# Kernel optimization log

Hardware: AMD Instinct MI355X
Metric: run time of the kernel (lower is better)

Reference implementation:

```python
import jax, jax.numpy as jnp
import numpy as np
from jax import lax

K = 2000      # node_num of GraphConvolution
H, W = 75, 100  # edge_region_feature spatial grid (from per-pixel concat loops)


def setup_inputs() -> dict:
    key = jax.random.key(0)
    k1, k2, k3, k4 = jax.random.split(key, 4)
    b, c = 8, 512
    edge_region_feature = jax.random.normal(k1, (b, c, H, W), dtype=jnp.float32)
    edge_region_predict = jax.random.normal(k2, (b, 3, H, W), dtype=jnp.float32)
    # GraphConvolution params: kaiming_normal_(fan_out) weights, zero bias
    w1 = jax.random.normal(k3, (512, 128), dtype=jnp.float32) * np.sqrt(2.0 / 128)
    b1 = jnp.zeros((K, 128), dtype=jnp.float32)
    w2 = jax.random.normal(k4, (128, 128), dtype=jnp.float32) * np.sqrt(2.0 / 128)
    b2 = jnp.zeros((K, 128), dtype=jnp.float32)
    return {"edge_region_feature": edge_region_feature,
            "edge_region_predict": edge_region_predict,
            "w1": w1, "b1": b1, "w2": w2, "b2": b2}


def reference(edge_region_feature, edge_region_predict, w1, b1, w2, b2):
    b, c = edge_region_feature.shape[0], edge_region_feature.shape[1]
    # block_feature built as: for x in range(W) for y in range(H) -> node n at (y=n%H, x=n//H)
    block = jnp.transpose(edge_region_feature, (0, 3, 2, 1)).reshape(b, W * H, c)  # (b, 7500, 512)

    # topk over channel-0 prediction, flattened row-major (idx = y*W + x)
    scores = edge_region_predict[:, 0, :, :].reshape(b, -1)            # (b, 7500)
    _vals, topk_idx = lax.top_k(scores, K)
    sorted_idx = jnp.sort(topk_idx, axis=1)                            # (b, 2000) int32

    # gather node features (replicates original's indexing of block_feature)
    node_map = jnp.take_along_axis(block, sorted_idx[:, :, None], axis=1)  # (b, 2000, 512)

    # generate_adjacent_map: decode positions with width=W, connect 8-neighborhood (+self)
    py = sorted_idx // W
    px = sorted_idx % W
    near_y = jnp.abs(py[:, :, None] - py[:, None, :]) <= 1
    near_x = jnp.abs(px[:, :, None] - px[:, None, :]) <= 1
    adj = (near_y & near_x).astype(jnp.float32)                        # (b, 2000, 2000)

    # node_feature_grouping = ReLU6 -> GCN(512->128) -> GCN(128->128)
    inp = jnp.clip(jnp.concatenate([adj, node_map], axis=2), 0.0, 6.0)  # ReLU6 on cat(adj, nodes)
    a = inp[:, :, :K]
    nf = inp[:, :, K:]
    # GCN1: A @ X @ W1 + b1  (in!=out -> no residual)
    x1 = jnp.einsum('bij,bjf->bif', a, nf) @ w1 + b1                   # (b, 2000, 128)
    # GCN2: A @ X1 @ W2 + b2 + X1 (in==out -> residual)
    x2 = jnp.einsum('bij,bjf->bif', a, x1) @ w2 + b2 + x1              # (b, 2000, 128)

    node_output_feature = jnp.tanh(x2)
    return node_output_feature, sorted_idx
```

## Files before the change

### kernel.cpp

```cpp
#include <hip/hip_runtime.h>
#include <cmath>

#define H_DIM 75
#define W_DIM 100
#define HW 7500
#define KSEL 2000
#define BATCH 8
#define CIN 512
#define FDIM 128

typedef short v4s __attribute__((ext_vector_type(4)));
typedef short v8s __attribute__((ext_vector_type(8)));
typedef float v16f __attribute__((ext_vector_type(16)));

__device__ __forceinline__ unsigned int map_key(float f) {
  unsigned int u = __float_as_uint(f);
  return (u & 0x80000000u) ? ~u : (u | 0x80000000u);
}

__device__ __forceinline__ float fast_tanh(float x) {
  float e = __expf(2.0f * x);
  return 1.0f - 2.0f * __builtin_amdgcn_rcpf(e + 1.0f);
}

__device__ __forceinline__ unsigned short bf16_rne(float v) {
  unsigned int u = __float_as_uint(v);
  unsigned int r = u + 0x7FFFu + ((u >> 16) & 1u);
  return (unsigned short)(r >> 16);
}
__device__ __forceinline__ float bf16_to_f(unsigned short h) {
  return __uint_as_float(((unsigned int)h) << 16);
}

__global__ __launch_bounds__(1024) void topk_nbr_kernel(
    const float* __restrict__ pred, const float* __restrict__ w1,
    const float* __restrict__ w2,
    int* __restrict__ off2_ws, int* __restrict__ perm_ws,
    float* __restrict__ out_idx,
    unsigned short* __restrict__ nbr, unsigned char* __restrict__ cnt,
    unsigned short* __restrict__ w1t_hi, unsigned short* __restrict__ w1t_lo,
    unsigned short* __restrict__ w2t_hi, unsigned short* __restrict__ w2t_lo)
{
  __shared__ unsigned int keys[HW];
  __shared__ unsigned int whist[16 * 256];
  __shared__ unsigned int hist[256];
  __shared__ unsigned int partials[16];
  __shared__ unsigned int s_prefix, s_kth;
  const int tid = threadIdx.x;

  if (blockIdx.x >= BATCH) {
    int base = (blockIdx.x - BATCH) * 1024 + tid;
    for (int e = base; e < CIN * FDIM + FDIM * FDIM; e += 8 * 1024) {
      if (e < CIN * FDIM) {
        int k = e & (CIN - 1), f = e >> 9;
        float v = w1[k * FDIM + f];
        unsigned short hi = bf16_rne(v);
        unsigned short lo = bf16_rne(v - bf16_to_f(hi));
        w1t_hi[(size_t)f * CIN + k] = hi;
        w1t_lo[(size_t)f * CIN + k] = lo;
      } else {
        int e2 = e - CIN * FDIM;
        int k = e2 & (FDIM - 1), f = e2 >> 7;
        float v = w2[k * FDIM + f];
        unsigned short hi = bf16_rne(v);
        unsigned short lo = bf16_rne(v - bf16_to_f(hi));
        w2t_hi[(size_t)f * FDIM + k] = hi;
        w2t_lo[(size_t)f * FDIM + k] = lo;
      }
    }
    return;
  }

  const int b = blockIdx.x;
  const int lane = tid & 63, w = tid >> 6;
  const float* scores = pred + (size_t)b * 3 * HW;
  for (int i = tid; i < HW; i += 1024) keys[i] = map_key(scores[i]);
  if (tid == 0) { s_prefix = 0u; s_kth = KSEL; }
  __syncthreads();

  for (int shift = 24; shift >= 0; shift -= 8) {
    for (int i = tid; i < 16 * 256; i += 1024) whist[i] = 0u;
    __syncthreads();
    unsigned int pref = s_prefix;
    unsigned int maskhi = (shift == 24) ? 0u : (0xFFFFFFFFu << (shift + 8));
    for (int i = tid; i < HW; i += 1024) {
      unsigned int k = keys[i];
      if ((k & maskhi) == pref)
        atomicAdd(&whist[w * 256 + ((k >> shift) & 0xFFu)], 1u);
    }
    __syncthreads();
    if (tid < 256) {
      unsigned int s = 0;
      #pragma unroll
      for (int ww = 0; ww < 16; ++ww) s += whist[ww * 256 + tid];
      hist[tid] = s;
    }
    __syncthreads();
    if (tid < 64) {
      unsigned int b0 = hist[tid * 4], b1 = hist[tid * 4 + 1];
      unsigned int b2 = hist[tid * 4 + 2], b3 = hist[tid * 4 + 3];
      unsigned int kth = s_kth;
      unsigned int T = b0 + b1 + b2 + b3;
      #pragma unroll
      for (int off = 1; off < 64; off <<= 1) {
        unsigned int t = __shfl_down(T, off, 64);
        if (tid + off < 64) T += t;
      }
      unsigned int U = __shfl_down(T, 1, 64);
      if (tid == 63) U = 0u;
      unsigned int s3 = b3 + U, s2 = b2 + s3, s1 = b1 + s2, s0 = b0 + s1;
      if (s0 >= kth && s1 < kth) { s_prefix = pref | ((unsigned)(4 * tid + 0) << shift); s_kth = kth - s1; }
      if (s1 >= kth && s2 < kth) { s_prefix = pref | ((unsigned)(4 * tid + 1) << shift); s_kth = kth - s2; }
      if (s2 >= kth && s3 < kth) { s_prefix = pref | ((unsigned)(4 * tid + 2) << shift); s_kth = kth - s3; }
      if (s3 >= kth && U  < kth) { s_prefix = pref | ((unsigned)(4 * tid + 3) << shift); s_kth = kth - U; }
    }
    __syncthreads();
  }
  const unsigned int thresh = s_prefix;

  unsigned int local[8];
  unsigned int sum = 0;
  #pragma unroll
  for (int e = 0; e < 8; ++e) {
    int i = tid * 8 + e;
    unsigned int p = 0;
    if (i < HW) {
      unsigned int ky = keys[i];
      if (ky > thresh) p = 1u;
      else if (ky == thresh) p = (1u << 16);
    }
    local[e] = p; sum += p;
  }
  __syncthreads();
  short* pos_of  = (short*)keys;
  int*   s_idx_sh = (int*)((char*)keys + 15000);
  for (int i = tid; i < HW; i += 1024) pos_of[i] = -1;

  unsigned int inc = sum;
  #pragma unroll
  for (int off = 1; off < 64; off <<= 1) {
    unsigned int t = __shfl_up(inc, off, 64);
    if (lane >= off) inc += t;
  }
  if (lane == 63) partials[w] = inc;
  __syncthreads();
  if (tid < 16) {
    unsigned int v = partials[tid];
    #pragma unroll
    for (int off = 1; off < 16; off <<= 1) {
      unsigned int t = __shfl_up(v, off, 64);
      if (tid >= off) v += t;
    }
    partials[tid] = v;
  }
  __syncthreads();
  unsigned int total = partials[15];
  unsigned int run = (w ? partials[w - 1] : 0u) + inc - sum;
  unsigned int ties = (unsigned int)KSEL - (total & 0xFFFFu);
  #pragma unroll
  for (int e = 0; e < 8; ++e) {
    int i = tid * 8 + e;
    unsigned int p = local[e];
    unsigned int gt_pref = run & 0xFFFFu;
    unsigned int eq_pref = run >> 16;
    bool sel = (p & 1u) || (((p >> 16) != 0u) && eq_pref < ties);
    if (sel) {
      unsigned int pos = gt_pref + (eq_pref < ties ? eq_pref : ties);
      out_idx[b * KSEL + pos] = (float)i;
      s_idx_sh[pos] = i;
      pos_of[i] = (short)pos;
    }
    run += p;
  }
  __syncthreads();

  if (tid < 128) hist[tid] = 0u;
  __syncthreads();
  for (int pos = tid; pos < KSEL; pos += 1024)
    atomicAdd(&hist[s_idx_sh[pos] % H_DIM], 1u);
  __syncthreads();
  if (tid == 0) {
    unsigned int run2 = 0u;
    for (int j = 0; j < H_DIM; ++j) { unsigned int t = hist[j]; hist[j] = run2; run2 += t; }
  }
  __syncthreads();
  for (int pos = tid; pos < KSEL; pos += 1024) {
    int i = s_idx_sh[pos];
    int y = i % H_DIM;
    unsigned int j = atomicAdd(&hist[y], 1u);
    off2_ws[b * KSEL + j] = (i % H_DIM) * W_DIM + i / H_DIM;
    perm_ws[b * KSEL + j] = pos;
  }

  for (int i = tid; i < KSEL; i += 1024) {
    int q = s_idx_sh[i];
    int py = q / W_DIM, px = q % W_DIM;
    unsigned short tmp[9];
    int c = 0;
    #pragma unroll
    for (int dy = -1; dy <= 1; ++dy) {
      int y = py + dy;
      if ((unsigned)y >= (unsigned)H_DIM) continue;
      #pragma unroll
      for (int dx = -1; dx <= 1; ++dx) {
        int x = px + dx;
        if ((unsigned)x >= (unsigned)W_DIM) continue;
        short p = pos_of[y * W_DIM + x];
        if (p >= 0) tmp[c++] = (unsigned short)p;
      }
    }
    #pragma unroll
    for (int t = 0; t < 9; ++t)
      nbr[(size_t)(b * KSEL + i) * 9 + t] = (t < c) ? tmp[t] : (unsigned short)0;
    cnt[b * KSEL + i] = (unsigned char)c;
  }
}

__global__ __launch_bounds__(256) void gemm1_fused(
    const float* __restrict__ feat, const int* __restrict__ off2_ws,
    const int* __restrict__ perm_ws,
    const unsigned short* __restrict__ w1t_hi,
    const unsigned short* __restrict__ w1t_lo,
    float* __restrict__ G)
{
  __shared__ unsigned short a_hi[3][64][20], a_lo[3][64][20];
  const int b = blockIdx.y;
  const int n0 = blockIdx.x * 64;
  const int tid = threadIdx.x;
  const int lane = tid & 63, w = tid >> 6;
  const int wr = w & 1, wc = w >> 1;
  const int q = lane >> 5, m = lane & 31;
  v16f acc0, acc1;
  #pragma unroll
  for (int i = 0; i < 16; ++i) { acc0[i] = 0.f; acc1[i] = 0.f; }
  const int an = wr * 32 + m;
  const int f0 = wc * 64 + m;
  const int n_st = tid & 63, ks = (tid >> 6) * 4;
  int nidx = n0 + n_st;
  if (nidx > KSEL - 1) nidx = KSEL - 1;
  const float* fb = feat + (size_t)b * CIN * HW + off2_ws[b * KSEL + nidx];

  float rv[3][4];
  #pragma unroll
  for (int s = 0; s < 3; ++s)
    #pragma unroll
    for (int j = 0; j < 4; ++j)
      rv[s][j] = fb[(size_t)(s * 16 + ks + j) * HW];
  #pragma unroll
  for (int j = 0; j < 4; ++j) {
    float v = fminf(fmaxf(rv[0][j], 0.f), 6.f);
    unsigned short hi = bf16_rne(v);
    a_hi[0][n_st][ks + j] = hi;
    a_lo[0][n_st][ks + j] = bf16_rne(v - bf16_to_f(hi));
  }

  #pragma unroll
  for (int i = 0; i < 32; ++i) {
    if (i + 1 < 32) {
      const int s = (i + 1) % 3;
      #pragma unroll
      for (int j = 0; j < 4; ++j) {
        float v = fminf(fmaxf(rv[s][j], 0.f), 6.f);
        unsigned short hi = bf16_rne(v);
        a_hi[s][n_st][ks + j] = hi;
        a_lo[s][n_st][ks + j] = bf16_rne(v - bf16_to_f(hi));
      }
      if (i + 3 < 32) {
        #pragma unroll
        for (int j = 0; j < 4; ++j)
          rv[s][j] = fb[(size_t)((i + 3) * 16 + ks + j) * HW];
      }
    }
    __syncthreads();
    const int p = i % 3;
    const int k0 = i * 16;
    v4s ah0 = *(const v4s*)&a_hi[p][an][q * 8];
    v4s ah1 = *(const v4s*)&a_hi[p][an][q * 8 + 4];
    v4s al0 = *(const v4s*)&a_lo[p][an][q * 8];
    v4s al1 = *(const v4s*)&a_lo[p][an][q * 8 + 4];
    v8s avh = __builtin_shufflevector(ah0, ah1, 0, 1, 2, 3, 4, 5, 6, 7);
    v8s avl = __builtin_shufflevector(al0, al1, 0, 1, 2, 3, 4, 5, 6, 7);
    v8s b0h = *(const v8s*)&w1t_hi[(size_t)f0 * CIN + k0 + q * 8];
    v8s b0l = *(const v8s*)&w1t_lo[(size_t)f0 * CIN + k0 + q * 8];
    v8s b1h = *(const v8s*)&w1t_hi[(size_t)(f0 + 32) * CIN + k0 + q * 8];
    v8s b1l = *(const v8s*)&w1t_lo[(size_t)(f0 + 32) * CIN + k0 + q * 8];
    acc0 = __builtin_amdgcn_mfma_f32_32x32x16_bf16(avh, b0h, acc0, 0, 0, 0);
    acc0 = __builtin_amdgcn_mfma_f32_32x32x16_bf16(avh, b0l, acc0, 0, 0, 0);
    acc0 = __builtin_amdgcn_mfma_f32_32x32x16_bf16(avl, b0h, acc0, 0, 0, 0);
    acc1 = __builtin_amdgcn_mfma_f32_32x32x16_bf16(avh, b1h, acc1, 0, 0, 0);
    acc1 = __builtin_amdgcn_mfma_f32_32x32x16_bf16(avh, b1l, acc1, 0, 0, 0);
    acc1 = __builtin_amdgcn_mfma_f32_32x32x16_bf16(avl, b1h, acc1, 0, 0, 0);
  }
  float* ob = G + (size_t)b * KSEL * FDIM;
  const int* pb = perm_ws + b * KSEL;
  #pragma unroll
  for (int reg = 0; reg < 16; ++reg) {
    int row = n0 + wr * 32 + (reg & 3) + 8 * (reg >> 2) + 4 * q;
    if (row < KSEL) {
      int pr = pb[row];
      ob[(size_t)pr * FDIM + f0]      = acc0[reg];
      ob[(size_t)pr * FDIM + f0 + 32] = acc1[reg];
    }
  }
}

__global__ __launch_bounds__(256) void gemm2_fused(
    const float* __restrict__ G, const float* __restrict__ b1,
    const unsigned short* __restrict__ nbr, const unsigned char* __restrict__ cnt,
    const unsigned short* __restrict__ w2t_hi,
    const unsigned short* __restrict__ w2t_lo,
    float* __restrict__ x1, float* __restrict__ Hm)
{
  __shared__ __align__(16) unsigned short xh[64][FDIM];
  __shared__ __align__(16) unsigned short xl[64][FDIM];
  const int b = blockIdx.y;
  const int n0 = blockIdx.x * 64;
  const int tid = threadIdx.x;
  const int g = tid >> 5, lane32 = tid & 31;
  const float4* G4 = (const float4*)G + (size_t)b * KSEL * 32;

  #pragma unroll 2
  for (int rr = 0; rr < 8; ++rr) {
    const int r = rr * 8 + g;
    const int node = n0 + r;
    const int nodec = (node > KSEL - 1) ? KSEL - 1 : node;
    const size_t bi = (size_t)b * KSEL + nodec;
    const unsigned short* nb = nbr + bi * 9;
    unsigned short idx[9];
    #pragma unroll
    for (int t = 0; t < 9; ++t) idx[t] = nb[t];
    const int c = cnt[bi];
    float4 v[9];
    #pragma unroll
    for (int t = 0; t < 9; ++t) v[t] = G4[(size_t)idx[t] * 32 + lane32];
    float4 acc = ((const float4*)b1)[nodec * 32 + lane32];
    #pragma unroll
    for (int t = 0; t < 9; ++t) {
      float mk = (t < c) ? 1.f : 0.f;
      acc.x = fmaf(v[t].x, mk, acc.x);
      acc.y = fmaf(v[t].y, mk, acc.y);
      acc.z = fmaf(v[t].z, mk, acc.z);
      acc.w = fmaf(v[t].w, mk, acc.w);
    }
    if (node < KSEL) ((float4*)x1)[bi * 32 + lane32] = acc;
    ushort4 h, l;
    h.x = bf16_rne(acc.x); l.x = bf16_rne(acc.x - bf16_to_f(h.x));
    h.y = bf16_rne(acc.y); l.y = bf16_rne(acc.y - bf16_to_f(h.y));
    h.z = bf16_rne(acc.z); l.z = bf16_rne(acc.z - bf16_to_f(h.z));
    h.w = bf16_rne(acc.w); l.w = bf16_rne(acc.w - bf16_to_f(h.w));
    const int cs = (lane32 * 4) ^ ((r & 15) << 3);
    *(ushort4*)&xh[r][cs] = h;
    *(ushort4*)&xl[r][cs] = l;
  }
  __syncthreads();

  const int lane = tid & 63, w = tid >> 6;
  const int wr = w & 1, wc = w >> 1;
  const int q = lane >> 5, m = lane & 31;
  const int ar = wr * 32 + m;
  const int f0 = wc * 64 + m;
  v16f acc0, acc1;
  #pragma unroll
  for (int i = 0; i < 16; ++i) { acc0[i] = 0.f; acc1[i] = 0.f; }
  #pragma unroll
  for (int k0 = 0; k0 < FDIM; k0 += 16) {
    const int ac = (k0 + q * 8) ^ ((ar & 15) << 3);
    v8s avh = *(const v8s*)&xh[ar][ac];
    v8s avl = *(const v8s*)&xl[ar][ac];
    v8s b0h = *(const v8s*)&w2t_hi[(size_t)f0 * FDIM + k0 + q * 8];
    v8s b0l = *(const v8s*)&w2t_lo[(size_t)f0 * FDIM + k0 + q * 8];
    v8s b1h = *(const v8s*)&w2t_hi[(size_t)(f0 + 32) * FDIM + k0 + q * 8];
    v8s b1l = *(const v8s*)&w2t_lo[(size_t)(f0 + 32) * FDIM + k0 + q * 8];
    acc0 = __builtin_amdgcn_mfma_f32_32x32x16_bf16(avh, b0h, acc0, 0, 0, 0);
    acc0 = __builtin_amdgcn_mfma_f32_32x32x16_bf16(avh, b0l, acc0, 0, 0, 0);
    acc0 = __builtin_amdgcn_mfma_f32_32x32x16_bf16(avl, b0h, acc0, 0, 0, 0);
    acc1 = __builtin_amdgcn_mfma_f32_32x32x16_bf16(avh, b1h, acc1, 0, 0, 0);
    acc1 = __builtin_amdgcn_mfma_f32_32x32x16_bf16(avh, b1l, acc1, 0, 0, 0);
    acc1 = __builtin_amdgcn_mfma_f32_32x32x16_bf16(avl, b1h, acc1, 0, 0, 0);
  }
  float* ob = Hm + (size_t)b * KSEL * FDIM;
  #pragma unroll
  for (int reg = 0; reg < 16; ++reg) {
    int row = n0 + wr * 32 + (reg & 3) + 8 * (reg >> 2) + 4 * q;
    if (row < KSEL) {
      ob[(size_t)row * FDIM + f0]      = acc0[reg];
      ob[(size_t)row * FDIM + f0 + 32] = acc1[reg];
    }
  }
}

__global__ __launch_bounds__(256) void out_kernel(
    const float* __restrict__ Hm, const float* __restrict__ x1,
    const float* __restrict__ b2,
    const unsigned short* __restrict__ nbr, const unsigned char* __restrict__ cnt,
    float* __restrict__ out)
{
  const int g = threadIdx.x >> 5, lane = threadIdx.x & 31;
  const int node = blockIdx.x * 8 + g;
  const int bb = blockIdx.y;
  const size_t bi = (size_t)bb * KSEL + node;
  const unsigned short* nb = nbr + bi * 9;
  unsigned short idx[9];
  #pragma unroll
  for (int t = 0; t < 9; ++t) idx[t] = nb[t];
  const int c = cnt[bi];
  const float4* H4 = (const float4*)Hm + (size_t)bb * KSEL * 32;
  float4 v[9];
  #pragma unroll
  for (int t = 0; t < 9; ++t) v[t] = H4[(size_t)idx[t] * 32 + lane];
  float4 acc = ((const float4*)b2)[node * 32 + lane];
  float4 xv = ((const float4*)x1)[bi * 32 + lane];
  acc.x += xv.x; acc.y += xv.y; acc.z += xv.z; acc.w += xv.w;
  #pragma unroll
  for (int t = 0; t < 9; ++t) {
    float mk = (t < c) ? 1.f : 0.f;
    acc.x = fmaf(v[t].x, mk, acc.x);
    acc.y = fmaf(v[t].y, mk, acc.y);
    acc.z = fmaf(v[t].z, mk, acc.z);
    acc.w = fmaf(v[t].w, mk, acc.w);
  }
  float4 r;
  r.x = fast_tanh(acc.x); r.y = fast_tanh(acc.y);
  r.z = fast_tanh(acc.z); r.w = fast_tanh(acc.w);
  ((float4*)out)[bi * 32 + lane] = r;
}

extern "C" void kernel_launch(void* const* d_in, const int* in_sizes, int n_in,
                              void* d_out, int out_size, void* d_ws, size_t ws_size,
                              hipStream_t stream) {
  const float* feat = (const float*)d_in[0];
  const float* pred = (const float*)d_in[1];
  const float* w1   = (const float*)d_in[2];
  const float* b1   = (const float*)d_in[3];
  const float* w2   = (const float*)d_in[4];
  const float* b2   = (const float*)d_in[5];
  float* out0 = (float*)d_out;
  float* out_idx = out0 + (size_t)BATCH * KSEL * FDIM;

  char* ws = (char*)d_ws;
  int*            off2_ws = (int*)(ws + 0);
  int*            perm_ws = (int*)(ws + 64256);
  unsigned short* nbr     = (unsigned short*)(ws + 128512);
  unsigned char*  cnt     = (unsigned char*)(ws + 416512);
  float*          G       = (float*)(ws + 432640);
  float*          x1      = (float*)(ws + 8624640);
  float*          Hm      = (float*)(ws + 16816640);
  unsigned short* w1t_hi  = (unsigned short*)(ws + 25008640);
  unsigned short* w1t_lo  = (unsigned short*)(ws + 25139712);
  unsigned short* w2t_hi  = (unsigned short*)(ws + 25270784);
  unsigned short* w2t_lo  = (unsigned short*)(ws + 25303552);

  topk_nbr_kernel<<<BATCH + 8, 1024, 0, stream>>>(
      pred, w1, w2, off2_ws, perm_ws, out_idx, nbr, cnt,
      w1t_hi, w1t_lo, w2t_hi, w2t_lo);
  gemm1_fused<<<dim3(32, BATCH), 256, 0, stream>>>(
      feat, off2_ws, perm_ws, w1t_hi, w1t_lo, G);
  gemm2_fused<<<dim3(32, BATCH), 256, 0, stream>>>(G, b1, nbr, cnt, w2t_hi, w2t_lo, x1, Hm);
  out_kernel<<<dim3(KSEL / 8, BATCH), 256, 0, stream>>>(Hm, x1, b2, nbr, cnt, out0);
}
```

Baseline: 233.5 us.

## Restructure gemm1 to single-wave blocks loading A fragments directly into registers

The gather GEMM now uses one 64-lane wave per block covering 32 nodes and all 128 output features. Each lane loads its A fragment straight from global memory into registers, with a 4-deep register prefetch. This removes the shared-memory staging and the per-iteration __syncthreads, and roughly doubles the block count (63x8 instead of 32x8) to spread work across more CUs. In exchange each wave holds four accumulators, raising register pressure, and each loaded feature value is converted to the hi/lo split only once per lane.

```diff
diff --git a/kernel.cpp b/kernel.cpp
--- a/kernel.cpp
+++ b/kernel.cpp
@@ -216,90 +216,71 @@
   }
 }
 
-__global__ __launch_bounds__(256) void gemm1_fused(
+__global__ __launch_bounds__(64) void gemm1_fused(
     const float* __restrict__ feat, const int* __restrict__ off2_ws,
     const int* __restrict__ perm_ws,
     const unsigned short* __restrict__ w1t_hi,
     const unsigned short* __restrict__ w1t_lo,
     float* __restrict__ G)
 {
-  __shared__ unsigned short a_hi[3][64][20], a_lo[3][64][20];
   const int b = blockIdx.y;
-  const int n0 = blockIdx.x * 64;
-  const int tid = threadIdx.x;
-  const int lane = tid & 63, w = tid >> 6;
-  const int wr = w & 1, wc = w >> 1;
+  const int n0 = blockIdx.x * 32;
+  const int lane = threadIdx.x;
   const int q = lane >> 5, m = lane & 31;
-  v16f acc0, acc1;
-  #pragma unroll
-  for (int i = 0; i < 16; ++i) { acc0[i] = 0.f; acc1[i] = 0.f; }
-  const int an = wr * 32 + m;
-  const int f0 = wc * 64 + m;
-  const int n_st = tid & 63, ks = (tid >> 6) * 4;
-  int nidx = n0 + n_st;
+  int nidx = n0 + m;
   if (nidx > KSEL - 1) nidx = KSEL - 1;
   const float* fb = feat + (size_t)b * CIN * HW + off2_ws[b * KSEL + nidx];
 
-  float rv[3][4];
-  #pragma unroll
-  for (int s = 0; s < 3; ++s)
-    #pragma unroll
-    for (int j = 0; j < 4; ++j)
-      rv[s][j] = fb[(size_t)(s * 16 + ks + j) * HW];
-  #pragma unroll
-  for (int j = 0; j < 4; ++j) {
-    float v = fminf(fmaxf(rv[0][j], 0.f), 6.f);
-    unsigned short hi = bf16_rne(v);
-    a_hi[0][n_st][ks + j] = hi;
-    a_lo[0][n_st][ks + j] = bf16_rne(v - bf16_to_f(hi));
-  }
+  v16f acc[4];
+  #pragma unroll
+  for (int c = 0; c < 4; ++c)
+    #pragma unroll
+    for (int i = 0; i < 16; ++i) acc[c][i] = 0.f;
+
+  float va[4][8];
+  #pragma unroll
+  for (int s = 0; s < 4; ++s)
+    #pragma unroll
+    for (int j = 0; j < 8; ++j)
+      va[s][j] = fb[(size_t)(s * 16 + q * 8 + j) * HW];
 
   #pragma unroll
   for (int i = 0; i < 32; ++i) {
-    if (i + 1 < 32) {
-      const int s = (i + 1) % 3;
+    const int s = i & 3;
+    v8s avh, avl;
+    #pragma unroll
+    for (int j = 0; j < 8; ++j) {
+      float v = fminf(fmaxf(va[s][j], 0.f), 6.f);
+      unsigned short hi = bf16_rne(v);
+      avh[j] = (short)hi;
+      avl[j] = (short)bf16_rne(v - bf16_to_f(hi));
+    }
+    if (i + 4 < 32) {
       #pragma unroll
-      for (int j = 0; j < 4; ++j) {
-        float v = fminf(fmaxf(rv[s][j], 0.f), 6.f);
-        unsigned short hi = bf16_rne(v);
-        a_hi[s][n_st][ks + j] = hi;
-        a_lo[s][n_st][ks + j] = bf16_rne(v - bf16_to_f(hi));
-      }
-      if (i + 3 < 32) {
-        #pragma unroll
-        for (int j = 0; j < 4; ++j)
-          rv[s][j] = fb[(size_t)((i + 3) * 16 + ks + j) * HW];
-      }
-    }
-    __syncthreads();
-    const int p = i % 3;
+      for (int j = 0; j < 8; ++j)
+        va[s][j] = fb[(size_t)((i + 4) * 16 + q * 8 + j) * HW];
+    }
     const int k0 = i * 16;
-    v4s ah0 = *(const v4s*)&a_hi[p][an][q * 8];
-    v4s ah1 = *(const v4s*)&a_hi[p][an][q * 8 + 4];
-    v4s al0 = *(const v4s*)&a_lo[p][an][q * 8];
-    v4s al1 = *(const v4s*)&a_lo[p][an][q * 8 + 4];
-    v8s avh = __builtin_shufflevector(ah0, ah1, 0, 1, 2, 3, 4, 5, 6, 7);
-    v8s avl = __builtin_shufflevector(al0, al1, 0, 1, 2, 3, 4, 5, 6, 7);
-    v8s b0h = *(const v8s*)&w1t_hi[(size_t)f0 * CIN + k0 + q * 8];
-    v8s b0l = *(const v8s*)&w1t_lo[(size_t)f0 * CIN + k0 + q * 8];
-    v8s b1h = *(const v8s*)&w1t_hi[(size_t)(f0 + 32) * CIN + k0 + q * 8];
-    v8s b1l = *(const v8s*)&w1t_lo[(size_t)(f0 + 32) * CIN + k0 + q * 8];
-    acc0 = __builtin_amdgcn_mfma_f32_32x32x16_bf16(avh, b0h, acc0, 0, 0, 0);
-    acc0 = __builtin_amdgcn_mfma_f32_32x32x16_bf16(avh, b0l, acc0, 0, 0, 0);
-    acc0 = __builtin_amdgcn_mfma_f32_32x32x16_bf16(avl, b0h, acc0, 0, 0, 0);
-    acc1 = __builtin_amdgcn_mfma_f32_32x32x16_bf16(avh, b1h, acc1, 0, 0, 0);
-    acc1 = __builtin_amdgcn_mfma_f32_32x32x16_bf16(avh, b1l, acc1, 0, 0, 0);
-    acc1 = __builtin_amdgcn_mfma_f32_32x32x16_bf16(avl, b1h, acc1, 0, 0, 0);
+    #pragma unroll
+    for (int c = 0; c < 4; ++c) {
+      const int f0 = c * 32 + m;
+      v8s bh = *(const v8s*)&w1t_hi[(size_t)f0 * CIN + k0 + q * 8];
+      v8s bl = *(const v8s*)&w1t_lo[(size_t)f0 * CIN + k0 + q * 8];
+      acc[c] = __builtin_amdgcn_mfma_f32_32x32x16_bf16(avh, bh, acc[c], 0, 0, 0);
+      acc[c] = __builtin_amdgcn_mfma_f32_32x32x16_bf16(avh, bl, acc[c], 0, 0, 0);
+      acc[c] = __builtin_amdgcn_mfma_f32_32x32x16_bf16(avl, bh, acc[c], 0, 0, 0);
+    }
   }
   float* ob = G + (size_t)b * KSEL * FDIM;
   const int* pb = perm_ws + b * KSEL;
   #pragma unroll
   for (int reg = 0; reg < 16; ++reg) {
-    int row = n0 + wr * 32 + (reg & 3) + 8 * (reg >> 2) + 4 * q;
+    int row = n0 + (reg & 3) + 8 * (reg >> 2) + 4 * q;
     if (row < KSEL) {
       int pr = pb[row];
-      ob[(size_t)pr * FDIM + f0]      = acc0[reg];
-      ob[(size_t)pr * FDIM + f0 + 32] = acc1[reg];
+      #pragma unroll
+      for (int c = 0; c < 4; ++c)
+        ob[(size_t)pr * FDIM + c * 32 + m] = acc[c][reg];
     }
   }
 }
@@ -453,7 +434,7 @@
   topk_nbr_kernel<<<BATCH + 8, 1024, 0, stream>>>(
       pred, w1, w2, off2_ws, perm_ws, out_idx, nbr, cnt,
       w1t_hi, w1t_lo, w2t_hi, w2t_lo);
-  gemm1_fused<<<dim3(32, BATCH), 256, 0, stream>>>(
+  gemm1_fused<<<dim3(63, BATCH), 64, 0, stream>>>(
       feat, off2_ws, perm_ws, w1t_hi, w1t_lo, G);
   gemm2_fused<<<dim3(32, BATCH), 256, 0, stream>>>(G, b1, nbr, cnt, w2t_hi, w2t_lo, x1, Hm);
   out_kernel<<<dim3(KSEL / 8, BATCH), 256, 0, stream>>>(Hm, x1, b2, nbr, cnt, out0);
```

After: 239.0 us. 1.02x slower.
